# Optimization experiments

Hardware: AMD Instinct MI355X
Metric: run time of the kernel (lower is better)

Reference implementation:

```python
import jax, jax.numpy as jnp
import numpy as np
import math

N_NODES = 30000
N_EDGES = 480000
MUL = 32            # multiplicity of 0e and 1o irreps
ATTR = 8            # node_attr dim (8x0e)
RAD = 8             # edge_scalars dim (8x0e radial basis)
FC_H = 64           # hidden width of radial MLP (fc_neurons)
N_PATHS = 4         # TP paths: s*Y0->0e, s*Y1->1o, v*Y0->1o, v.Y1->0e
N_LAYERS = 3
AVG_DEG = 16.0
LOG2 = math.log(2.0)


def ssp(x):
    # shifted softplus
    return jax.nn.softplus(x) - LOG2


def setup_inputs() -> dict:
    key = jax.random.key(0)
    ks = jax.random.split(key, 16)
    inp = {
        'node_input': jax.random.normal(ks[0], (N_NODES, 4 * MUL), dtype=jnp.float32),
        'node_attr': jax.random.uniform(ks[1], (N_NODES, ATTR), dtype=jnp.float32),
        'edge_src': jax.random.randint(ks[2], (N_EDGES,), 0, N_NODES),
        'edge_dst': jax.random.randint(ks[3], (N_EDGES,), 0, N_NODES),
        'edge_attr': jax.random.normal(ks[4], (N_EDGES, 4), dtype=jnp.float32),
        'edge_scalars': jax.random.normal(ks[5], (N_EDGES, RAD), dtype=jnp.float32),
        # per-layer stacked params (leading dim = N_LAYERS)
        'lin1_s': jax.random.normal(ks[6], (N_LAYERS, MUL, MUL), dtype=jnp.float32),
        'lin1_v': jax.random.normal(ks[7], (N_LAYERS, MUL, MUL), dtype=jnp.float32),
        'mlp_w1': jax.random.normal(ks[8], (N_LAYERS, RAD, FC_H), dtype=jnp.float32),
        'mlp_w2': jax.random.normal(ks[9], (N_LAYERS, FC_H, FC_H), dtype=jnp.float32),
        'mlp_w3': jax.random.normal(ks[10], (N_LAYERS, FC_H, N_PATHS * MUL), dtype=jnp.float32),
        'lin2_s': jax.random.normal(ks[11], (N_LAYERS, 2 * MUL, 2 * MUL), dtype=jnp.float32),
        'lin2_v': jax.random.normal(ks[12], (N_LAYERS, 2 * MUL, MUL), dtype=jnp.float32),
        'sc_s': jax.random.normal(ks[13], (N_LAYERS, MUL, ATTR, 2 * MUL), dtype=jnp.float32),
        'sc_v': jax.random.normal(ks[14], (N_LAYERS, MUL, ATTR, MUL), dtype=jnp.float32),
    }
    return inp


def _layer(x, node_attr, edge_src, edge_dst, Y, edge_scalars,
           lin1_s, lin1_v, w1, w2, w3, lin2_s, lin2_v, sc_s, sc_v):
    n = x.shape[0]
    s = x[:, :MUL]                         # [N, 32]   0e
    v = x[:, MUL:].reshape(n, MUL, 3)      # [N, 32, 3] 1o

    # self-connection: fully-connected TP (node x node_attr -> conv_out)
    sc_norm = 1.0 / math.sqrt(MUL * ATTR)
    sc_sa = jnp.einsum('nu,na,uaw->nw', s, node_attr, sc_s) * sc_norm      # [N, 64]
    sc_va = jnp.einsum('nuc,na,uaw->nwc', v, node_attr, sc_v) * sc_norm    # [N, 32, 3]

    # lin1 (mixes channels within each irrep)
    s1 = (s @ lin1_s) / math.sqrt(MUL)
    v1 = jnp.einsum('nuc,uw->nwc', v, lin1_v) / math.sqrt(MUL)

    # radial MLP -> per-edge, per-path, per-channel TP weights
    h = ssp((edge_scalars @ w1) / math.sqrt(RAD))
    h = ssp((h @ w2) / math.sqrt(FC_H))
    w = ((h @ w3) / math.sqrt(FC_H)).reshape(-1, N_PATHS, MUL)  # [E, 4, 32]

    # gather source node features
    se = s1[edge_src]                      # [E, 32]
    ve = v1[edge_src]                      # [E, 32, 3]
    Y0 = Y[:, :1]                          # [E, 1]  l=0 sh
    Y1 = Y[:, 1:]                          # [E, 3]  l=1 sh

    # channelwise (uvu) tensor product paths
    m_s1 = w[:, 0] * se * Y0                                   # 0e x 0e -> 0e
    m_s2 = w[:, 3] * jnp.einsum('euc,ec->eu', ve, Y1)          # 1o x 1o -> 0e
    m_v1 = (w[:, 1] * se)[:, :, None] * Y1[:, None, :]         # 0e x 1o -> 1o
    m_v2 = w[:, 2][:, :, None] * ve * Y0[:, :, None]           # 1o x 0e -> 1o

    msg = jnp.concatenate(
        [m_s1, m_s2, m_v1.reshape(-1, 3 * MUL), m_v2.reshape(-1, 3 * MUL)], axis=-1
    )  # [E, 256]

    agg = jax.ops.segment_sum(msg, edge_dst, num_segments=n) / math.sqrt(AVG_DEG)
    a_s = agg[:, : 2 * MUL]                       # [N, 64]
    a_v = agg[:, 2 * MUL:].reshape(n, 2 * MUL, 3) # [N, 64, 3]

    # lin2 + self-connection
    out_s = (a_s @ lin2_s) / math.sqrt(2 * MUL) + sc_sa                     # [N, 64]
    out_v = jnp.einsum('nuc,uw->nwc', a_v, lin2_v) / math.sqrt(2 * MUL) + sc_va  # [N, 32, 3]

    # Gate: scalars ssp, gates ssp, vectors * gates
    scalars = ssp(out_s[:, :MUL])
    gates = ssp(out_s[:, MUL:])
    gated = out_v * gates[:, :, None]
    out = jnp.concatenate([scalars, gated.reshape(n, 3 * MUL)], axis=-1)

    return x + out  # resnet (irreps match every layer)


def reference(node_input, node_attr, edge_src, edge_dst, edge_attr, edge_scalars,
              lin1_s, lin1_v, mlp_w1, mlp_w2, mlp_w3, lin2_s, lin2_v, sc_s, sc_v):
    x = node_input
    for i in range(N_LAYERS):
        x = _layer(x, node_attr, edge_src, edge_dst, edge_attr, edge_scalars,
                   lin1_s[i], lin1_v[i], mlp_w1[i], mlp_w2[i], mlp_w3[i],
                   lin2_s[i], lin2_v[i], sc_s[i], sc_v[i])
    return x
```

## Files before the change

kernel.cpp:

```cpp
#include <hip/hip_runtime.h>
#include <math.h>

#define N_NODES 30000
#define N_EDGES 480000

typedef __attribute__((ext_vector_type(8))) short s8v;
typedef __attribute__((ext_vector_type(4))) float f4v;

__device__ inline unsigned short f2bf(float f) {
  union { float f; unsigned u; } v; v.f = f;
  return (unsigned short)((v.u + 0x7fffu + ((v.u >> 16) & 1u)) >> 16);
}
__device__ inline float bfh2f(unsigned short h) {
  union { unsigned u; float f; } v; v.u = (unsigned)h << 16; return v.f;
}
__device__ inline float sspf(float x) {
  float t = __expf(-fabsf(x));
  return fmaxf(x, 0.f) + __logf(1.f + t) - 0.69314718055994531f;
}

__global__ __launch_bounds__(256) void k_hist(const int* __restrict__ edst, int* __restrict__ counts) {
  int e = blockIdx.x * 256 + threadIdx.x;
  if (e < N_EDGES) atomicAdd(&counts[edst[e]], 1);
}

#define SCAN_T 1024
#define NPER 30
__global__ __launch_bounds__(1024) void k_scan(const int* __restrict__ counts,
                                               int* __restrict__ row_start, int* __restrict__ cursor) {
  __shared__ int part[SCAN_T];
  int t = threadIdx.x;
  int base = t * NPER;
  int local[NPER];
  int s = 0;
#pragma unroll
  for (int j = 0; j < NPER; ++j) {
    int idx = base + j;
    int c = (idx < N_NODES) ? counts[idx] : 0;
    local[j] = s;
    s += c;
  }
  part[t] = s;
  __syncthreads();
  for (int off = 1; off < SCAN_T; off <<= 1) {
    int v = (t >= off) ? part[t - off] : 0;
    __syncthreads();
    part[t] += v;
    __syncthreads();
  }
  int pre = (t == 0) ? 0 : part[t - 1];
#pragma unroll
  for (int j = 0; j < NPER; ++j) {
    int idx = base + j;
    if (idx < N_NODES) {
      int v = pre + local[j];
      row_start[idx] = v;
      cursor[idx] = v;
    }
  }
  if (t == SCAN_T - 1) row_start[N_NODES] = pre + s;
}

__global__ __launch_bounds__(256) void k_scatter(const int* __restrict__ edst,
                                                 int* __restrict__ cursor, int* __restrict__ eidx) {
  int e = blockIdx.x * 256 + threadIdx.x;
  if (e < N_EDGES) {
    int pos = atomicAdd(&cursor[edst[e]], 1);
    eidx[pos] = e;
  }
}

__global__ __launch_bounds__(256) void k_sortseg(const int* __restrict__ row_start, int* __restrict__ eidx) {
  int n = blockIdx.x * 256 + threadIdx.x;
  if (n >= N_NODES) return;
  int jb = row_start[n], je = row_start[n + 1];
  for (int i = jb + 1; i < je; ++i) {
    int v = eidx[i];
    int j = i - 1;
    while (j >= jb && eidx[j] > v) { eidx[j + 1] = eidx[j]; --j; }
    eidx[j + 1] = v;
  }
}

__global__ __launch_bounds__(256) void k_node_pre(const float* __restrict__ x,
    const float* __restrict__ l1s, const float* __restrict__ l1v,
    float* __restrict__ s1v1)
{
  int t = blockIdx.x * 256 + threadIdx.x;
  int node = t >> 7, j = t & 127;
  const float* xr = x + (size_t)node * 128;
  float acc = 0.f;
  if (j < 32) {
#pragma unroll
    for (int u = 0; u < 32; ++u) acc += xr[u] * l1s[u * 32 + j];
  } else {
    int jj = j - 32, m = jj / 3, c = jj - 3 * m;
#pragma unroll
    for (int u = 0; u < 32; ++u) acc += xr[32 + u * 3 + c] * l1v[u * 32 + m];
  }
  s1v1[t] = acc * 0.17677669529663689f;
}

__global__ __launch_bounds__(256, 3) void k_edge_agg(
    const float* __restrict__ esc, const int* __restrict__ esrc,
    const float* __restrict__ eattr, const float* __restrict__ s1v1,
    const int* __restrict__ row_start, const int* __restrict__ eidx,
    const float* __restrict__ w1g, const float* __restrict__ w2g, const float* __restrict__ w3g,
    float* __restrict__ agg)
{
  __shared__ __attribute__((aligned(16))) unsigned short W2T[64 * 72];
  __shared__ __attribute__((aligned(16))) unsigned short W3T[128 * 72];
  __shared__ __attribute__((aligned(16))) unsigned short Hb[4][2][16 * 72];

  const int tid = threadIdx.x, lane = tid & 63, wv = tid >> 6;
  const int c0 = lane & 15, g = lane >> 4;

  for (int idx = tid; idx < 64 * 64; idx += 256) {
    int k = idx >> 6, n2 = idx & 63;
    W2T[n2 * 72 + k] = f2bf(w2g[idx]);
  }
  for (int idx = tid; idx < 64 * 128; idx += 256) {
    int k = idx >> 7, n2 = idx & 127;
    W3T[n2 * 72 + k] = f2bf(w3g[idx]);
  }
  s8v B1[4];
#pragma unroll
  for (int nt = 0; nt < 4; ++nt)
#pragma unroll
    for (int i = 0; i < 8; ++i) {
      float w = w1g[i * 64 + nt * 16 + c0];
      unsigned short hi = f2bf(w);
      B1[nt][i] = (g < 2) ? (short)hi : (short)f2bf(w - bfh2f(hi));
    }
  __syncthreads();

  unsigned short* hhi = &Hb[wv][0][0];
  unsigned short* hlo = &Hb[wv][1][0];
  const f4v z = {0.f, 0.f, 0.f, 0.f};

  const int node = blockIdx.x * 4 + wv;
  const int jb = row_start[node], je = row_start[node + 1];

  float nacc[16];
#pragma unroll
  for (int k = 0; k < 16; ++k) nacc[k] = 0.f;

  for (int base = jb; base < je; base += 16) {
    const int nvalid = je - base;
    s8v A1 = {0, 0, 0, 0, 0, 0, 0, 0};
    if (c0 < nvalid) {
      int eid = eidx[base + c0];
      const float4* p = (const float4*)(esc + (size_t)eid * 8);
      float4 a = p[0], b = p[1];
      float e8[8] = {a.x, a.y, a.z, a.w, b.x, b.y, b.z, b.w};
#pragma unroll
      for (int j = 0; j < 8; ++j) {
        unsigned short hi = f2bf(e8[j]);
        A1[j] = (g & 1) ? (short)f2bf(e8[j] - bfh2f(hi)) : (short)hi;
      }
    }
#pragma unroll
    for (int nt = 0; nt < 4; ++nt) {
      f4v acc = __builtin_amdgcn_mfma_f32_16x16x32_bf16(A1, B1[nt], z, 0, 0, 0);
#pragma unroll
      for (int i = 0; i < 4; ++i) {
        float hv = sspf(acc[i] * 0.35355339059327373f);
        unsigned short hi = f2bf(hv);
        hhi[(g * 4 + i) * 72 + nt * 16 + c0] = hi;
        hlo[(g * 4 + i) * 72 + nt * 16 + c0] = f2bf(hv - bfh2f(hi));
      }
    }
    s8v A2ah = *(const s8v*)&hhi[c0 * 72 + 8 * g];
    s8v A2bh = *(const s8v*)&hhi[c0 * 72 + 32 + 8 * g];
    s8v A2al = *(const s8v*)&hlo[c0 * 72 + 8 * g];
    s8v A2bl = *(const s8v*)&hlo[c0 * 72 + 32 + 8 * g];
#pragma unroll
    for (int nt = 0; nt < 4; ++nt) {
      s8v Ba = *(const s8v*)&W2T[(nt * 16 + c0) * 72 + 8 * g];
      s8v Bb = *(const s8v*)&W2T[(nt * 16 + c0) * 72 + 32 + 8 * g];
      f4v acc = __builtin_amdgcn_mfma_f32_16x16x32_bf16(A2ah, Ba, z, 0, 0, 0);
      acc = __builtin_amdgcn_mfma_f32_16x16x32_bf16(A2bh, Bb, acc, 0, 0, 0);
      acc = __builtin_amdgcn_mfma_f32_16x16x32_bf16(A2al, Ba, acc, 0, 0, 0);
      acc = __builtin_amdgcn_mfma_f32_16x16x32_bf16(A2bl, Bb, acc, 0, 0, 0);
#pragma unroll
      for (int i = 0; i < 4; ++i) {
        float hv = sspf(acc[i] * 0.125f);
        unsigned short hi = f2bf(hv);
        hhi[(g * 4 + i) * 72 + nt * 16 + c0] = hi;
        hlo[(g * 4 + i) * 72 + nt * 16 + c0] = f2bf(hv - bfh2f(hi));
      }
    }
    s8v A3ah = *(const s8v*)&hhi[c0 * 72 + 8 * g];
    s8v A3bh = *(const s8v*)&hhi[c0 * 72 + 32 + 8 * g];
    s8v A3al = *(const s8v*)&hlo[c0 * 72 + 8 * g];
    s8v A3bl = *(const s8v*)&hlo[c0 * 72 + 32 + 8 * g];
    f4v acc3[8];
#pragma unroll
    for (int nt = 0; nt < 8; ++nt) {
      s8v Ba = *(const s8v*)&W3T[(nt * 16 + c0) * 72 + 8 * g];
      s8v Bb = *(const s8v*)&W3T[(nt * 16 + c0) * 72 + 32 + 8 * g];
      acc3[nt] = __builtin_amdgcn_mfma_f32_16x16x32_bf16(A3ah, Ba, z, 0, 0, 0);
      acc3[nt] = __builtin_amdgcn_mfma_f32_16x16x32_bf16(A3bh, Bb, acc3[nt], 0, 0, 0);
      acc3[nt] = __builtin_amdgcn_mfma_f32_16x16x32_bf16(A3al, Ba, acc3[nt], 0, 0, 0);
      acc3[nt] = __builtin_amdgcn_mfma_f32_16x16x32_bf16(A3bl, Bb, acc3[nt], 0, 0, 0);
    }
    float msg[16];
#pragma unroll
    for (int k = 0; k < 16; ++k) msg[k] = 0.f;
#pragma unroll
    for (int i = 0; i < 4; ++i) {
      int s = g * 4 + i;
      float w0 = acc3[0][i] * 0.125f, w1_ = acc3[1][i] * 0.125f;
      float w2_ = acc3[2][i] * 0.125f, w3_ = acc3[3][i] * 0.125f;
      float w4_ = acc3[4][i] * 0.125f, w5_ = acc3[5][i] * 0.125f;
      float w6_ = acc3[6][i] * 0.125f, w7_ = acc3[7][i] * 0.125f;
      if (s < nvalid) {
        int eid = eidx[base + s];
        int src = esrc[eid];
        float4 y = *(const float4*)(eattr + (size_t)eid * 4);
        const float* svp = s1v1 + (size_t)src * 128;
        float sA = svp[c0], sB = svp[c0 + 16];
        float vA0 = svp[32 + 3 * c0], vA1 = svp[33 + 3 * c0], vA2 = svp[34 + 3 * c0];
        float vB0 = svp[80 + 3 * c0], vB1 = svp[81 + 3 * c0], vB2 = svp[82 + 3 * c0];
        msg[0] += w0 * sA * y.x;
        msg[1] += w1_ * sB * y.x;
        msg[2] += w6_ * (vA0 * y.y + vA1 * y.z + vA2 * y.w);
        msg[3] += w7_ * (vB0 * y.y + vB1 * y.z + vB2 * y.w);
        msg[4] += w2_ * sA * y.y;  msg[5] += w2_ * sA * y.z;  msg[6] += w2_ * sA * y.w;
        msg[7] += w3_ * sB * y.y;  msg[8] += w3_ * sB * y.z;  msg[9] += w3_ * sB * y.w;
        msg[10] += w4_ * vA0 * y.x; msg[11] += w4_ * vA1 * y.x; msg[12] += w4_ * vA2 * y.x;
        msg[13] += w5_ * vB0 * y.x; msg[14] += w5_ * vB1 * y.x; msg[15] += w5_ * vB2 * y.x;
      }
    }
#pragma unroll
    for (int k = 0; k < 16; ++k) {
      float v = msg[k];
      v += __shfl_xor(v, 16, 64);
      v += __shfl_xor(v, 32, 64);
      nacc[k] += v;
    }
  }
  if (g == 0) {
    float* ad = agg + (size_t)node * 256;
    ad[c0] = nacc[0];
    ad[16 + c0] = nacc[1];
    ad[32 + c0] = nacc[2];
    ad[48 + c0] = nacc[3];
#pragma unroll
    for (int c = 0; c < 3; ++c) {
      ad[64 + 3 * c0 + c]  = nacc[4 + c];
      ad[112 + 3 * c0 + c] = nacc[7 + c];
      ad[160 + 3 * c0 + c] = nacc[10 + c];
      ad[208 + 3 * c0 + c] = nacc[13 + c];
    }
  }
}

__global__ __launch_bounds__(256) void k_node_post(
    const float* __restrict__ x, const float* __restrict__ attr, const float* __restrict__ agg,
    const float* __restrict__ l2s, const float* __restrict__ l2v,
    const float* __restrict__ scs, const float* __restrict__ scv,
    float* __restrict__ out)
{
  __shared__ float xa[4][4][136];
  __shared__ float ag[4][4][256];
  const int l = threadIdx.x & 63, wv = threadIdx.x >> 6;
  const int n0 = blockIdx.x * 16 + wv * 4;
#pragma unroll
  for (int b = 0; b < 4; ++b) {
    int nd = n0 + b;
    xa[wv][b][l] = x[(size_t)nd * 128 + l];
    xa[wv][b][64 + l] = x[(size_t)nd * 128 + 64 + l];
    if (l < 8) xa[wv][b][128 + l] = attr[nd * 8 + l];
#pragma unroll
    for (int q = 0; q < 4; ++q) ag[wv][b][q * 64 + l] = agg[(size_t)nd * 256 + q * 64 + l];
  }
  float attr_r[4][8];
#pragma unroll
  for (int b = 0; b < 4; ++b)
#pragma unroll
    for (int a = 0; a < 8; ++a) attr_r[b][a] = xa[wv][b][128 + a];

  const int w1 = l / 3, c1 = l - 3 * w1;
  const int f2 = 64 + l;
  const int w2r = f2 / 3, c2r = f2 - 3 * w2r;
  const int w2 = (l < 32) ? w2r : 0, c2 = (l < 32) ? c2r : 0;

  float acc[4] = {0.f, 0.f, 0.f, 0.f}, sa[4] = {0.f, 0.f, 0.f, 0.f};
  float av1[4] = {0.f, 0.f, 0.f, 0.f}, sv1[4] = {0.f, 0.f, 0.f, 0.f};
  float av2[4] = {0.f, 0.f, 0.f, 0.f}, sv2[4] = {0.f, 0.f, 0.f, 0.f};

#pragma unroll 8
  for (int u = 0; u < 64; ++u) {
    float wl = l2s[u * 64 + l];
#pragma unroll
    for (int b = 0; b < 4; ++b) acc[b] += ag[wv][b][u] * wl;
  }
#pragma unroll 4
  for (int u = 0; u < 64; ++u) {
    float wla = l2v[u * 32 + w1];
    float wlb = l2v[u * 32 + w2];
#pragma unroll
    for (int b = 0; b < 4; ++b) {
      av1[b] += ag[wv][b][64 + 3 * u + c1] * wla;
      av2[b] += ag[wv][b][64 + 3 * u + c2] * wlb;
    }
  }
  for (int u = 0; u < 32; ++u) {
    float sb[4];
#pragma unroll
    for (int b = 0; b < 4; ++b) sb[b] = xa[wv][b][u];
#pragma unroll
    for (int a = 0; a < 8; ++a) {
      float wl = scs[(u * 8 + a) * 64 + l];
#pragma unroll
      for (int b = 0; b < 4; ++b) sa[b] += sb[b] * attr_r[b][a] * wl;
    }
  }
  for (int u = 0; u < 32; ++u) {
    float vb1[4], vb2[4];
#pragma unroll
    for (int b = 0; b < 4; ++b) {
      vb1[b] = xa[wv][b][32 + 3 * u + c1];
      vb2[b] = xa[wv][b][32 + 3 * u + c2];
    }
#pragma unroll
    for (int a = 0; a < 8; ++a) {
      float wla = scv[(u * 8 + a) * 32 + w1];
      float wlb = scv[(u * 8 + a) * 32 + w2];
#pragma unroll
      for (int b = 0; b < 4; ++b) {
        sv1[b] += vb1[b] * attr_r[b][a] * wla;
        sv2[b] += vb2[b] * attr_r[b][a] * wlb;
      }
    }
  }

#pragma unroll
  for (int b = 0; b < 4; ++b) {
    float outs = acc[b] * 0.03125f + sa[b] * 0.0625f;
    float gss = sspf(outs);
    float ov1 = av1[b] * 0.03125f + sv1[b] * 0.0625f;
    float ov2 = av2[b] * 0.03125f + sv2[b] * 0.0625f;
    float gate1 = __shfl(gss, 32 + w1, 64);
    float gate2 = __shfl(gss, 32 + w2, 64);
    float* o = out + (size_t)(n0 + b) * 128;
    if (l < 32) o[l] = xa[wv][b][l] + gss;
    o[32 + l] = xa[wv][b][32 + l] + ov1 * gate1;
    if (l < 32) o[96 + l] = xa[wv][b][96 + l] + ov2 * gate2;
  }
}

extern "C" void kernel_launch(void* const* d_in, const int* in_sizes, int n_in,
                              void* d_out, int out_size, void* d_ws, size_t ws_size,
                              hipStream_t stream) {
  const float* node_input = (const float*)d_in[0];
  const float* node_attr  = (const float*)d_in[1];
  const int*   esrc  = (const int*)d_in[2];
  const int*   edst  = (const int*)d_in[3];
  const float* eattr = (const float*)d_in[4];
  const float* escal = (const float*)d_in[5];
  const float* l1s = (const float*)d_in[6];
  const float* l1v = (const float*)d_in[7];
  const float* w1  = (const float*)d_in[8];
  const float* w2  = (const float*)d_in[9];
  const float* w3  = (const float*)d_in[10];
  const float* l2s = (const float*)d_in[11];
  const float* l2v = (const float*)d_in[12];
  const float* scs = (const float*)d_in[13];
  const float* scv = (const float*)d_in[14];
  float* out  = (float*)d_out;

  float* s1v1 = (float*)d_ws;
  float* agg  = s1v1 + (size_t)N_NODES * 128;
  int* counts    = (int*)(agg + (size_t)N_NODES * 256);
  int* row_start = counts + N_NODES;
  int* cursor    = row_start + N_NODES + 1;
  int* eidx      = cursor + N_NODES;

  hipMemsetAsync(counts, 0, (size_t)N_NODES * sizeof(int), stream);
  k_hist<<<(N_EDGES + 255) / 256, 256, 0, stream>>>(edst, counts);
  k_scan<<<1, SCAN_T, 0, stream>>>(counts, row_start, cursor);
  k_scatter<<<(N_EDGES + 255) / 256, 256, 0, stream>>>(edst, cursor, eidx);
  k_sortseg<<<(N_NODES + 255) / 256, 256, 0, stream>>>(row_start, eidx);

  for (int layer = 0; layer < 3; ++layer) {
    const float* xin = (layer == 0) ? node_input : (const float*)out;
    k_node_pre<<<N_NODES * 128 / 256, 256, 0, stream>>>(
        xin, l1s + layer * 1024, l1v + layer * 1024, s1v1);
    k_edge_agg<<<N_NODES / 4, 256, 0, stream>>>(escal, esrc, eattr, s1v1,
        row_start, eidx, w1 + layer * 512, w2 + layer * 4096, w3 + layer * 8192, agg);
    k_node_post<<<N_NODES / 16, 256, 0, stream>>>(xin, node_attr, agg,
        l2s + layer * 4096, l2v + layer * 2048, scs + layer * 16384, scv + layer * 8192, out);
  }
}
```

Measured before the change: 1.340 ms.

## Materialize dst-sorted edge data, interleave node features, warp-bitonic segment sort

Replaces the per-thread insertion sort of each node's edge list with a wavefront bitonic sort for degrees up to 64. A new pass writes edge-sorted copies of source ids, edge attributes and the pre-split bf16 hi/lo radial features, so the edge kernel reads them contiguously instead of through eidx indirection. s1v1 is stored in a per-lane interleaved layout so each lane fetches its eight gathered values as two float4 loads, and these loads are issued before the third MLP stage to overlap latency. It needs extra workspace and falls back to the old path when the workspace is too small.

```diff
diff --git a/kernel.cpp b/kernel.cpp
--- a/kernel.cpp
+++ b/kernel.cpp
@@ -71,15 +71,54 @@
 }
 
 __global__ __launch_bounds__(256) void k_sortseg(const int* __restrict__ row_start, int* __restrict__ eidx) {
-  int n = blockIdx.x * 256 + threadIdx.x;
-  if (n >= N_NODES) return;
-  int jb = row_start[n], je = row_start[n + 1];
-  for (int i = jb + 1; i < je; ++i) {
-    int v = eidx[i];
-    int j = i - 1;
-    while (j >= jb && eidx[j] > v) { eidx[j + 1] = eidx[j]; --j; }
-    eidx[j + 1] = v;
-  }
+  int wid = (blockIdx.x * 256 + threadIdx.x) >> 6;
+  int lane = threadIdx.x & 63;
+  if (wid >= N_NODES) return;
+  int jb = row_start[wid], je = row_start[wid + 1];
+  int deg = je - jb;
+  if (deg <= 1) return;
+  if (deg <= 64) {
+    int key = (lane < deg) ? eidx[jb + lane] : 0x7fffffff;
+#pragma unroll
+    for (int k = 2; k <= 64; k <<= 1) {
+      for (int j = k >> 1; j > 0; j >>= 1) {
+        int other = __shfl_xor(key, j, 64);
+        bool asc = ((lane & k) == 0);
+        bool upper = ((lane & j) != 0);
+        key = (upper == asc) ? max(key, other) : min(key, other);
+      }
+    }
+    if (lane < deg) eidx[jb + lane] = key;
+  } else if (lane == 0) {
+    for (int i = jb + 1; i < je; ++i) {
+      int v = eidx[i];
+      int j = i - 1;
+      while (j >= jb && eidx[j] > v) { eidx[j + 1] = eidx[j]; --j; }
+      eidx[j + 1] = v;
+    }
+  }
+}
+
+__global__ __launch_bounds__(256) void k_mat(const int* __restrict__ eidx, const int* __restrict__ esrc,
+    const float* __restrict__ esc, const float* __restrict__ eattr,
+    unsigned short* __restrict__ esc_hl, float4* __restrict__ y_s, int* __restrict__ src_s) {
+  int p = blockIdx.x * 256 + threadIdx.x;
+  if (p >= N_EDGES) return;
+  int e = eidx[p];
+  src_s[p] = esrc[e];
+  y_s[p] = *(const float4*)(eattr + (size_t)e * 4);
+  const float4* q = (const float4*)(esc + (size_t)e * 8);
+  float4 a = q[0], b = q[1];
+  float e8[8] = {a.x, a.y, a.z, a.w, b.x, b.y, b.z, b.w};
+  s8v hi, lo;
+#pragma unroll
+  for (int j = 0; j < 8; ++j) {
+    unsigned short h = f2bf(e8[j]);
+    hi[j] = (short)h;
+    lo[j] = (short)f2bf(e8[j] - bfh2f(h));
+  }
+  *(s8v*)(esc_hl + (size_t)p * 16) = hi;
+  *(s8v*)(esc_hl + (size_t)p * 16 + 8) = lo;
 }
 
 __global__ __launch_bounds__(256) void k_node_pre(const float* __restrict__ x,
@@ -88,23 +127,28 @@
 {
   int t = blockIdx.x * 256 + threadIdx.x;
   int node = t >> 7, j = t & 127;
+  int slot = j >> 3, r = j & 7;
   const float* xr = x + (size_t)node * 128;
   float acc = 0.f;
-  if (j < 32) {
-#pragma unroll
-    for (int u = 0; u < 32; ++u) acc += xr[u] * l1s[u * 32 + j];
+  if (r < 2) {
+    int m = slot + 16 * r;
+#pragma unroll
+    for (int u = 0; u < 32; ++u) acc += xr[u] * l1s[u * 32 + m];
   } else {
-    int jj = j - 32, m = jj / 3, c = jj - 3 * m;
+    int q = r - 2;
+    int m = slot + ((q >= 3) ? 16 : 0);
+    int c = q % 3;
 #pragma unroll
     for (int u = 0; u < 32; ++u) acc += xr[32 + u * 3 + c] * l1v[u * 32 + m];
   }
   s1v1[t] = acc * 0.17677669529663689f;
 }
 
+template<int MAT>
 __global__ __launch_bounds__(256, 3) void k_edge_agg(
-    const float* __restrict__ esc, const int* __restrict__ esrc,
-    const float* __restrict__ eattr, const float* __restrict__ s1v1,
-    const int* __restrict__ row_start, const int* __restrict__ eidx,
+    const float* __restrict__ esc, const int* __restrict__ esrc, const float* __restrict__ eattr,
+    const unsigned short* __restrict__ esc_hl, const int* __restrict__ src_s, const float4* __restrict__ y_s,
+    const float* __restrict__ s1v1, const int* __restrict__ row_start, const int* __restrict__ eidx,
     const float* __restrict__ w1g, const float* __restrict__ w2g, const float* __restrict__ w3g,
     float* __restrict__ agg)
 {
@@ -148,15 +192,41 @@
   for (int base = jb; base < je; base += 16) {
     const int nvalid = je - base;
     s8v A1 = {0, 0, 0, 0, 0, 0, 0, 0};
-    if (c0 < nvalid) {
-      int eid = eidx[base + c0];
-      const float4* p = (const float4*)(esc + (size_t)eid * 8);
-      float4 a = p[0], b = p[1];
-      float e8[8] = {a.x, a.y, a.z, a.w, b.x, b.y, b.z, b.w};
-#pragma unroll
-      for (int j = 0; j < 8; ++j) {
-        unsigned short hi = f2bf(e8[j]);
-        A1[j] = (g & 1) ? (short)f2bf(e8[j] - bfh2f(hi)) : (short)hi;
+    int srcv[4];
+    float4 yv[4];
+    bool val[4];
+    if constexpr (MAT) {
+      if (c0 < nvalid)
+        A1 = *(const s8v*)(esc_hl + (size_t)(base + c0) * 16 + (size_t)(g & 1) * 8);
+#pragma unroll
+      for (int i = 0; i < 4; ++i) {
+        int s = g * 4 + i;
+        val[i] = (s < nvalid);
+        srcv[i] = 0; yv[i] = make_float4(0.f, 0.f, 0.f, 0.f);
+        if (val[i]) { srcv[i] = src_s[base + s]; yv[i] = y_s[base + s]; }
+      }
+    } else {
+      if (c0 < nvalid) {
+        int eid = eidx[base + c0];
+        const float4* p = (const float4*)(esc + (size_t)eid * 8);
+        float4 a = p[0], b = p[1];
+        float e8[8] = {a.x, a.y, a.z, a.w, b.x, b.y, b.z, b.w};
+#pragma unroll
+        for (int j = 0; j < 8; ++j) {
+          unsigned short hi = f2bf(e8[j]);
+          A1[j] = (g & 1) ? (short)f2bf(e8[j] - bfh2f(hi)) : (short)hi;
+        }
+      }
+#pragma unroll
+      for (int i = 0; i < 4; ++i) {
+        int s = g * 4 + i;
+        val[i] = (s < nvalid);
+        srcv[i] = 0; yv[i] = make_float4(0.f, 0.f, 0.f, 0.f);
+        if (val[i]) {
+          int eid = eidx[base + s];
+          srcv[i] = esrc[eid];
+          yv[i] = *(const float4*)(eattr + (size_t)eid * 4);
+        }
       }
     }
 #pragma unroll
@@ -190,6 +260,18 @@
         hlo[(g * 4 + i) * 72 + nt * 16 + c0] = f2bf(hv - bfh2f(hi));
       }
     }
+    float4 pr0[4], pr1[4];
+#pragma unroll
+    for (int i = 0; i < 4; ++i) {
+      if (val[i]) {
+        const float* svp = s1v1 + (size_t)srcv[i] * 128 + c0 * 8;
+        pr0[i] = *(const float4*)svp;
+        pr1[i] = *(const float4*)(svp + 4);
+      } else {
+        pr0[i] = make_float4(0.f, 0.f, 0.f, 0.f);
+        pr1[i] = make_float4(0.f, 0.f, 0.f, 0.f);
+      }
+    }
     s8v A3ah = *(const s8v*)&hhi[c0 * 72 + 8 * g];
     s8v A3bh = *(const s8v*)&hhi[c0 * 72 + 32 + 8 * g];
     s8v A3al = *(const s8v*)&hlo[c0 * 72 + 8 * g];
@@ -209,19 +291,15 @@
     for (int k = 0; k < 16; ++k) msg[k] = 0.f;
 #pragma unroll
     for (int i = 0; i < 4; ++i) {
-      int s = g * 4 + i;
       float w0 = acc3[0][i] * 0.125f, w1_ = acc3[1][i] * 0.125f;
       float w2_ = acc3[2][i] * 0.125f, w3_ = acc3[3][i] * 0.125f;
       float w4_ = acc3[4][i] * 0.125f, w5_ = acc3[5][i] * 0.125f;
       float w6_ = acc3[6][i] * 0.125f, w7_ = acc3[7][i] * 0.125f;
-      if (s < nvalid) {
-        int eid = eidx[base + s];
-        int src = esrc[eid];
-        float4 y = *(const float4*)(eattr + (size_t)eid * 4);
-        const float* svp = s1v1 + (size_t)src * 128;
-        float sA = svp[c0], sB = svp[c0 + 16];
-        float vA0 = svp[32 + 3 * c0], vA1 = svp[33 + 3 * c0], vA2 = svp[34 + 3 * c0];
-        float vB0 = svp[80 + 3 * c0], vB1 = svp[81 + 3 * c0], vB2 = svp[82 + 3 * c0];
+      if (val[i]) {
+        float4 y = yv[i];
+        float sA = pr0[i].x, sB = pr0[i].y;
+        float vA0 = pr0[i].z, vA1 = pr0[i].w, vA2 = pr1[i].x;
+        float vB0 = pr1[i].y, vB1 = pr1[i].z, vB2 = pr1[i].w;
         msg[0] += w0 * sA * y.x;
         msg[1] += w1_ * sB * y.x;
         msg[2] += w6_ * (vA0 * y.y + vA1 * y.z + vA2 * y.w);
@@ -371,25 +449,38 @@
   const float* scv = (const float*)d_in[14];
   float* out  = (float*)d_out;
 
-  float* s1v1 = (float*)d_ws;
-  float* agg  = s1v1 + (size_t)N_NODES * 128;
-  int* counts    = (int*)(agg + (size_t)N_NODES * 256);
+  char* p = (char*)d_ws;
+  float* s1v1 = (float*)p;                 p += (size_t)N_NODES * 128 * 4;
+  float* agg  = (float*)p;                 p += (size_t)N_NODES * 256 * 4;
+  int* eidx   = (int*)p;                   p += (size_t)N_EDGES * 4;
+  unsigned short* esc_hl = (unsigned short*)p;  p += (size_t)N_EDGES * 16 * 2;
+  float4* y_s = (float4*)p;                p += (size_t)N_EDGES * 16;
+  int* src_s  = (int*)p;                   p += (size_t)N_EDGES * 4;
+  size_t need_mat = (size_t)(p - (char*)d_ws) + (size_t)(N_NODES * 2 + 1) * 4;
+  char* tail = ((size_t)ws_size >= need_mat) ? p : (char*)(eidx + N_EDGES);
+  int* counts    = (int*)tail;
   int* row_start = counts + N_NODES;
   int* cursor    = row_start + N_NODES + 1;
-  int* eidx      = cursor + N_NODES;
+  const bool use_mat = ((size_t)ws_size >= need_mat);
 
   hipMemsetAsync(counts, 0, (size_t)N_NODES * sizeof(int), stream);
   k_hist<<<(N_EDGES + 255) / 256, 256, 0, stream>>>(edst, counts);
   k_scan<<<1, SCAN_T, 0, stream>>>(counts, row_start, cursor);
   k_scatter<<<(N_EDGES + 255) / 256, 256, 0, stream>>>(edst, cursor, eidx);
-  k_sortseg<<<(N_NODES + 255) / 256, 256, 0, stream>>>(row_start, eidx);
+  k_sortseg<<<(N_NODES * 64 + 255) / 256, 256, 0, stream>>>(row_start, eidx);
+  if (use_mat)
+    k_mat<<<(N_EDGES + 255) / 256, 256, 0, stream>>>(eidx, esrc, escal, eattr, esc_hl, y_s, src_s);
 
   for (int layer = 0; layer < 3; ++layer) {
     const float* xin = (layer == 0) ? node_input : (const float*)out;
     k_node_pre<<<N_NODES * 128 / 256, 256, 0, stream>>>(
         xin, l1s + layer * 1024, l1v + layer * 1024, s1v1);
-    k_edge_agg<<<N_NODES / 4, 256, 0, stream>>>(escal, esrc, eattr, s1v1,
-        row_start, eidx, w1 + layer * 512, w2 + layer * 4096, w3 + layer * 8192, agg);
+    if (use_mat)
+      k_edge_agg<1><<<N_NODES / 4, 256, 0, stream>>>(escal, esrc, eattr, esc_hl, src_s, y_s,
+          s1v1, row_start, eidx, w1 + layer * 512, w2 + layer * 4096, w3 + layer * 8192, agg);
+    else
+      k_edge_agg<0><<<N_NODES / 4, 256, 0, stream>>>(escal, esrc, eattr, esc_hl, src_s, y_s,
+          s1v1, row_start, eidx, w1 + layer * 512, w2 + layer * 4096, w3 + layer * 8192, agg);
     k_node_post<<<N_NODES / 16, 256, 0, stream>>>(xin, node_attr, agg,
         l2s + layer * 4096, l2v + layer * 2048, scs + layer * 16384, scv + layer * 8192, out);
   }
```

After: 1.507 ms. 12.5% more time.
